# Kernel tuning notes

Hardware: AMD Instinct MI355X
Metric: run time of the kernel (lower is better)

Reference implementation:

```python
import jax, jax.numpy as jnp
import numpy as np

DIM = 384
HEADS = 6
HIDDEN = int(DIM * 4.0)
SQRT_2_OVER_PI = float(np.sqrt(2.0 / np.pi))
LN_EPS = 1e-5


def gelu_tanh(x):
    return 0.5 * x * (1.0 + jnp.tanh(SQRT_2_OVER_PI * (x + 0.044715 * x ** 3)))


def layer_norm(x, g, b):
    m = jnp.mean(x, axis=-1, keepdims=True)
    v = jnp.var(x, axis=-1, keepdims=True)
    return (x - m) * jax.lax.rsqrt(v + LN_EPS) * g + b


def setup_inputs() -> dict:
    key = jax.random.key(0)
    ks = jax.random.split(key, 8)
    s = 0.02
    return {
        "x": jax.random.normal(ks[0], (4, 2048, DIM), dtype=jnp.float32),
        "ln1_g": jnp.ones((DIM,), jnp.float32),
        "ln1_b": jnp.zeros((DIM,), jnp.float32),
        "w_qkv": jax.random.normal(ks[1], (DIM, 3 * DIM), jnp.float32) * s,
        "w_proj": jax.random.normal(ks[2], (DIM, DIM), jnp.float32) * s,
        "b_proj": jnp.zeros((DIM,), jnp.float32),
        "ln2_g": jnp.ones((DIM,), jnp.float32),
        "ln2_b": jnp.zeros((DIM,), jnp.float32),
        "w_fc1": jax.random.normal(ks[3], (DIM, HIDDEN), jnp.float32) * s,
        "b_fc1": jnp.zeros((HIDDEN,), jnp.float32),
        "w_fc2": jax.random.normal(ks[4], (HIDDEN, DIM), jnp.float32) * s,
        "b_fc2": jnp.zeros((DIM,), jnp.float32),
    }


def reference(x, ln1_g, ln1_b, w_qkv, w_proj, b_proj, ln2_g, ln2_b, w_fc1, b_fc1, w_fc2, b_fc2):
    B, N, C = x.shape
    H = HEADS
    Dh = C // H
    scale = Dh ** -0.5

    # Attention (pre-norm)
    h = layer_norm(x, ln1_g, ln1_b)
    qkv = (h @ w_qkv).reshape(B, N, 3, H, Dh)
    q = qkv[:, :, 0].transpose(0, 2, 1, 3)  # [B,H,N,Dh]
    k = qkv[:, :, 1].transpose(0, 2, 1, 3)
    v = qkv[:, :, 2].transpose(0, 2, 1, 3)
    attn = jnp.einsum('bhnd,bhmd->bhnm', q, k) * scale
    attn = jax.nn.softmax(attn, axis=-1)
    o = jnp.einsum('bhnm,bhmd->bhnd', attn, v)
    o = o.transpose(0, 2, 1, 3).reshape(B, N, C)
    x = x + (o @ w_proj + b_proj)

    # MLP (pre-norm)
    h = layer_norm(x, ln2_g, ln2_b)
    h = gelu_tanh(h @ w_fc1 + b_fc1)
    x = x + (h @ w_fc2 + b_fc2)
    return x
```

## Files before the change

### kernel.cpp

```cpp
#include <hip/hip_runtime.h>
#include <hip/hip_bf16.h>
#include <math.h>

#define DIM 384
#define HEADS 6
#define DH 64
#define HIDDEN 1536
#define SEQ 2048
#define NTOK 8192
#define LN_EPS 1e-5f
#define S2PI 0.7978845608028654f
#define KPAD 72

typedef __attribute__((ext_vector_type(8))) short short8;
typedef __attribute__((ext_vector_type(4))) float f32x4;
typedef __attribute__((ext_vector_type(4))) unsigned short ushort4v;
typedef __attribute__((ext_vector_type(8))) unsigned short ushort8v;

#if __has_builtin(__builtin_amdgcn_exp2f)
#define EXP2(x) __builtin_amdgcn_exp2f(x)
#else
#define EXP2(x) exp2f(x)
#endif
#if __has_builtin(__builtin_amdgcn_rcpf)
#define RCPF(x) __builtin_amdgcn_rcpf(x)
#else
#define RCPF(x) (1.f / (x))
#endif

__device__ __forceinline__ unsigned short f2bf(float f) {
    union { float f; unsigned u; } v; v.f = f;
    unsigned r = v.u + 0x7FFFu + ((v.u >> 16) & 1u);
    return (unsigned short)(r >> 16);
}

__device__ __forceinline__ float bf2f(unsigned short u) {
    union { unsigned u; float f; } v; v.u = ((unsigned)u) << 16;
    return v.f;
}

__device__ __forceinline__ float gelu_fast(float v) {
    float u = S2PI * (v + 0.044715f * v * v * v);
    float e = EXP2(u * 2.8853900817779268f);
    return v * (1.f - RCPF(1.f + e));
}

__device__ __forceinline__ void gload16(const unsigned short* g, unsigned short* l) {
    __builtin_amdgcn_global_load_lds(
        (const __attribute__((address_space(1))) unsigned int*)g,
        (__attribute__((address_space(3))) unsigned int*)l, 16, 0, 0);
}

__device__ __forceinline__ void ln_body(const float* __restrict__ x,
                                        const float* __restrict__ g,
                                        const float* __restrict__ b,
                                        unsigned short* __restrict__ out,
                                        int blk, int tid) {
    int row  = blk * 4 + (tid >> 6);
    int lane = tid & 63;
    const float* xr = x + (size_t)row * DIM;
    float v[6];
    float s = 0.f, sq = 0.f;
#pragma unroll
    for (int j = 0; j < 6; ++j) {
        v[j] = xr[lane + 64 * j];
        s += v[j];
        sq += v[j] * v[j];
    }
#pragma unroll
    for (int o = 32; o; o >>= 1) {
        s  += __shfl_xor(s, o);
        sq += __shfl_xor(sq, o);
    }
    float mean = s * (1.f / DIM);
    float var  = sq * (1.f / DIM) - mean * mean;
    float rs   = rsqrtf(var + LN_EPS);
    unsigned short* orow = out + (size_t)row * DIM;
#pragma unroll
    for (int j = 0; j < 6; ++j) {
        int c = lane + 64 * j;
        orow[c] = f2bf((v[j] - mean) * rs * g[c] + b[c]);
    }
}

__device__ __forceinline__ void tr_body(const float* __restrict__ w,
                                        unsigned short* __restrict__ wt,
                                        int K, int N, int bx, int by,
                                        unsigned short (*t)[36], int tid) {
    const int n0 = bx * 32, k0 = by * 32;
    {
        int r = tid >> 3, c4 = (tid & 7) * 4;
        float4 v = *reinterpret_cast<const float4*>(&w[(size_t)(k0 + r) * N + n0 + c4]);
        t[c4 + 0][r] = f2bf(v.x);
        t[c4 + 1][r] = f2bf(v.y);
        t[c4 + 2][r] = f2bf(v.z);
        t[c4 + 3][r] = f2bf(v.w);
    }
    __syncthreads();
    {
        int n = tid >> 3, kk = (tid & 7) * 4;
        ushort4v o = { t[n][kk], t[n][kk + 1], t[n][kk + 2], t[n][kk + 3] };
        *reinterpret_cast<ushort4v*>(&wt[(size_t)(n0 + n) * K + k0 + kk]) = o;
    }
}

__global__ __launch_bounds__(256) void prep_kernel(const float* __restrict__ x,
                                                   const float* __restrict__ g1,
                                                   const float* __restrict__ b1,
                                                   unsigned short* __restrict__ h_bf,
                                                   const float* __restrict__ w_qkv,
                                                   unsigned short* __restrict__ wqkv_t,
                                                   const float* __restrict__ w_proj,
                                                   unsigned short* __restrict__ wproj_t,
                                                   const float* __restrict__ w_fc1,
                                                   unsigned short* __restrict__ wfc1_t,
                                                   const float* __restrict__ w_fc2,
                                                   unsigned short* __restrict__ wfc2_t) {
    __shared__ unsigned short t[32][36];
    const int tid = threadIdx.x;
    int bid = blockIdx.x;
    if (bid < 2048) { ln_body(x, g1, b1, h_bf, bid, tid); return; }
    bid -= 2048;
    if (bid < 432) { tr_body(w_qkv, wqkv_t, DIM, 3 * DIM, bid % 36, bid / 36, t, tid); return; }
    bid -= 432;
    if (bid < 144) { tr_body(w_proj, wproj_t, DIM, DIM, bid % 12, bid / 12, t, tid); return; }
    bid -= 144;
    if (bid < 576) { tr_body(w_fc1, wfc1_t, DIM, HIDDEN, bid % 48, bid / 48, t, tid); return; }
    bid -= 576;
    tr_body(w_fc2, wfc2_t, HIDDEN, DIM, bid % 12, bid / 12, t, tid);
}

__global__ __launch_bounds__(256) void ln_kernel(const float* __restrict__ x,
                                                 const float* __restrict__ g,
                                                 const float* __restrict__ b,
                                                 unsigned short* __restrict__ out) {
    ln_body(x, g, b, out, blockIdx.x, threadIdx.x);
}

template <int EPI, int BN>
__global__ __launch_bounds__(256) void mfma_gemm(const unsigned short* __restrict__ A,
                                                 const unsigned short* __restrict__ Bt,
                                                 const float* __restrict__ bias,
                                                 const float* __restrict__ resid,
                                                 float* __restrict__ Cf,
                                                 unsigned short* __restrict__ Cb,
                                                 unsigned short* __restrict__ Qh,
                                                 unsigned short* __restrict__ Kh,
                                                 unsigned short* __restrict__ Vth,
                                                 int M, int N, int K) {
    constexpr int NF = BN / 32;
    __shared__ __align__(16) unsigned short smem[EPI == 0 ? 17408 : (128 * 64 + BN * 64)];
    unsigned short* As = smem;
    unsigned short* Bs = smem + 128 * 64;

    const int tid = threadIdx.x;
    const int wave = tid >> 6, lane = tid & 63;
    const int lg = lane >> 4, lrr = lane & 15;
    const int wr = wave >> 1, wc = wave & 1;
    const int bm = blockIdx.y * 128, bn = blockIdx.x * BN;

    f32x4 acc[4][NF];
    const f32x4 fzero = {0.f, 0.f, 0.f, 0.f};
#pragma unroll
    for (int m = 0; m < 4; ++m)
#pragma unroll
        for (int n = 0; n < NF; ++n) acc[m][n] = fzero;

    const int grow = wave * 8 + (lane >> 3);
    const int gcol = (lane & 7) * 8;
    const unsigned short* apl = A  + (size_t)(bm + grow) * K + gcol;
    const unsigned short* bpl = Bt + (size_t)(bn + grow) * K + gcol;

    for (int k0 = 0; k0 < K; k0 += 64) {
        __syncthreads();
#pragma unroll
        for (int i = 0; i < 4; ++i)
            gload16(apl + (size_t)(i * 32) * K + k0, As + i * 2048 + wave * 512);
#pragma unroll
        for (int i = 0; i < NF; ++i)
            gload16(bpl + (size_t)(i * 32) * K + k0, Bs + i * 2048 + wave * 512);
        __syncthreads();
#pragma unroll
        for (int s = 0; s < 2; ++s) {
            short8 af[4], bf[NF];
#pragma unroll
            for (int m = 0; m < 4; ++m)
                af[m] = *reinterpret_cast<const short8*>(
                    &As[(wr * 64 + m * 16 + lrr) * 64 + s * 32 + lg * 8]);
#pragma unroll
            for (int n = 0; n < NF; ++n)
                bf[n] = *reinterpret_cast<const short8*>(
                    &Bs[(wc * (BN / 2) + n * 16 + lrr) * 64 + s * 32 + lg * 8]);
#pragma unroll
            for (int m = 0; m < 4; ++m)
#pragma unroll
                for (int n = 0; n < NF; ++n)
                    acc[m][n] = __builtin_amdgcn_mfma_f32_16x16x32_bf16(af[m], bf[n], acc[m][n], 0, 0, 0);
        }
    }

    if (EPI == 1) {
#pragma unroll
        for (int m = 0; m < 4; ++m)
#pragma unroll
            for (int j = 0; j < 4; ++j) {
                int row = bm + wr * 64 + m * 16 + lg * 4 + j;
#pragma unroll
                for (int n = 0; n < NF; ++n) {
                    int col = bn + wc * (BN / 2) + n * 16 + lrr;
                    size_t off = (size_t)row * N + col;
                    Cf[off] = acc[m][n][j] + bias[col] + resid[off];
                }
            }
    } else if (EPI == 2) {
#pragma unroll
        for (int m = 0; m < 4; ++m)
#pragma unroll
            for (int j = 0; j < 4; ++j) {
                int row = bm + wr * 64 + m * 16 + lg * 4 + j;
#pragma unroll
                for (int n = 0; n < NF; ++n) {
                    int col = bn + wc * (BN / 2) + n * 16 + lrr;
                    Cb[(size_t)row * N + col] = f2bf(gelu_fast(acc[m][n][j] + bias[col]));
                }
            }
    } else {
        const int sec = bn / DIM;
        if (sec < 2) {
            unsigned short* dst = (sec == 0) ? Qh : Kh;
#pragma unroll
            for (int m = 0; m < 4; ++m)
#pragma unroll
                for (int j = 0; j < 4; ++j) {
                    int token = bm + wr * 64 + m * 16 + lg * 4 + j;
                    int bb = token >> 11, nn = token & (SEQ - 1);
#pragma unroll
                    for (int n = 0; n < NF; ++n) {
                        int n_glob = bn + wc * (BN / 2) + n * 16 + lrr;
                        int head = (n_glob - sec * DIM) >> 6;
                        int d = n_glob & 63;
                        dst[((size_t)(bb * HEADS + head) * SEQ + nn) * DH + d] =
                            f2bf(acc[m][n][j]);
                    }
                }
        } else {
            __syncthreads();
            unsigned short* T = smem;
#pragma unroll
            for (int m = 0; m < 4; ++m)
#pragma unroll
                for (int n = 0; n < NF; ++n) {
                    int dl = wc * (BN / 2) + n * 16 + lrr;
#pragma unroll
                    for (int j = 0; j < 4; ++j) {
                        int tl = wr * 64 + m * 16 + lg * 4 + j;
                        T[dl * 136 + tl] = f2bf(acc[m][n][j]);
                    }
                }
            __syncthreads();
            int dl = tid >> 1, th = (tid & 1) * 64;
            int dg = bn - 2 * DIM + dl;
            int head = dg >> 6, dd = dg & 63;
            int bb = bm >> 11, nn0 = (bm & (SEQ - 1)) + th;
            unsigned short* dst = &Vth[((size_t)(bb * HEADS + head) * DH + dd) * SEQ + nn0];
#pragma unroll
            for (int i = 0; i < 64; i += 8)
                *reinterpret_cast<ushort8v*>(dst + i) =
                    *reinterpret_cast<const ushort8v*>(&T[dl * 136 + th + i]);
        }
    }
}

__global__ __launch_bounds__(256) void attn_mfma_kernel(const unsigned short* __restrict__ Qh,
                                                        const unsigned short* __restrict__ Kh,
                                                        const unsigned short* __restrict__ Vth,
                                                        unsigned short* __restrict__ out) {
    const int bid = blockIdx.x;
    const int orig = (bid & 7) * 96 + (bid >> 3);
    const int qt = orig & 31;
    const int bh = orig >> 5;
    const int b = bh / HEADS, h = bh % HEADS;
    const int tid = threadIdx.x;
    const int wave = tid >> 6, lane = tid & 63;
    const int lg = lane >> 4;
    const int lrr = lane & 15;

    __shared__ __align__(16) unsigned short Ks[64][KPAD];
    __shared__ __align__(16) unsigned short Vs[64][KPAD];
    __shared__ __align__(16) unsigned short Ps[4][16][KPAD];

    const size_t qkbase = (size_t)bh * SEQ * DH;
    const size_t vbase  = (size_t)bh * DH * SEQ;

    short8 qfrag[2];
    {
        const unsigned short* qp =
            Qh + qkbase + (size_t)(qt * 64 + wave * 16 + lrr) * DH + lg * 8;
        qfrag[0] = *(const short8*)qp;
        qfrag[1] = *(const short8*)(qp + 32);
#pragma unroll
        for (int s = 0; s < 2; ++s)
#pragma unroll
            for (int i = 0; i < 8; ++i)
                qfrag[s][i] = (short)f2bf(bf2f((unsigned short)qfrag[s][i]) * 0.18033688011112042f);
    }

    float lsum = 0.f;
    f32x4 oacc[4];
    const f32x4 fzero = {0.f, 0.f, 0.f, 0.f};
#pragma unroll
    for (int n = 0; n < 4; ++n) oacc[n] = fzero;

    const int sr = tid >> 2;
    const int sc = (tid & 3) * 16;

    const unsigned short* kp = Kh + qkbase + (size_t)sr * DH + sc;
    const unsigned short* vp = Vth + vbase + (size_t)sr * SEQ + sc;
    short8 rk0 = *(const short8*)kp;
    short8 rk1 = *(const short8*)(kp + 8);
    short8 rv0 = *(const short8*)vp;
    short8 rv1 = *(const short8*)(vp + 8);

    const int NT = SEQ / 64;
    for (int kt = 0; kt < NT; ++kt) {
        *(short8*)&Ks[sr][sc]     = rk0;
        *(short8*)&Ks[sr][sc + 8] = rk1;
        *(short8*)&Vs[sr][sc]     = rv0;
        *(short8*)&Vs[sr][sc + 8] = rv1;
        if (kt + 1 < NT) {
            kp += 64 * DH;
            vp += 64;
            rk0 = *(const short8*)kp;
            rk1 = *(const short8*)(kp + 8);
            rv0 = *(const short8*)vp;
            rv1 = *(const short8*)(vp + 8);
        }
        asm volatile("s_waitcnt lgkmcnt(0)" ::: "memory");
        __builtin_amdgcn_s_barrier();
        __builtin_amdgcn_sched_barrier(0);

        f32x4 sacc[4];
#pragma unroll
        for (int ct = 0; ct < 4; ++ct) sacc[ct] = fzero;
        __builtin_amdgcn_s_setprio(1);
#pragma unroll
        for (int ct = 0; ct < 4; ++ct) {
#pragma unroll
            for (int s = 0; s < 2; ++s) {
                short8 kf = *(const short8*)&Ks[ct * 16 + lrr][s * 32 + lg * 8];
                sacc[ct] = __builtin_amdgcn_mfma_f32_16x16x32_bf16(kf, qfrag[s], sacc[ct], 0, 0, 0);
            }
        }
        __builtin_amdgcn_s_setprio(0);

#pragma unroll
        for (int ct = 0; ct < 4; ++ct) {
            float p0 = EXP2(sacc[ct][0]);
            float p1 = EXP2(sacc[ct][1]);
            float p2 = EXP2(sacc[ct][2]);
            float p3 = EXP2(sacc[ct][3]);
            lsum += (p0 + p1) + (p2 + p3);
            union { __hip_bfloat162 h2; unsigned u; } w0, w1;
            w0.h2 = __float22bfloat162_rn(float2{p0, p1});
            w1.h2 = __float22bfloat162_rn(float2{p2, p3});
            unsigned long long dw = (unsigned long long)w0.u |
                                    ((unsigned long long)w1.u << 32);
            *reinterpret_cast<unsigned long long*>(&Ps[wave][lrr][ct * 16 + lg * 4]) = dw;
        }

        short8 pf0 = *(const short8*)&Ps[wave][lrr][lg * 8];
        short8 pf1 = *(const short8*)&Ps[wave][lrr][32 + lg * 8];
        __builtin_amdgcn_s_setprio(1);
#pragma unroll
        for (int n = 0; n < 4; ++n) {
            short8 vf0 = *(const short8*)&Vs[n * 16 + lrr][lg * 8];
            oacc[n] = __builtin_amdgcn_mfma_f32_16x16x32_bf16(pf0, vf0, oacc[n], 0, 0, 0);
            short8 vf1 = *(const short8*)&Vs[n * 16 + lrr][32 + lg * 8];
            oacc[n] = __builtin_amdgcn_mfma_f32_16x16x32_bf16(pf1, vf1, oacc[n], 0, 0, 0);
        }
        __builtin_amdgcn_s_setprio(0);
        __builtin_amdgcn_s_barrier();
    }

    float ls = lsum;
    ls += __shfl_xor(ls, 16);
    ls += __shfl_xor(ls, 32);
    float linv = 1.f / ls;

    const int orow0 = qt * 64 + wave * 16 + lg * 4;
#pragma unroll
    for (int j = 0; j < 4; ++j) {
        float inv = __shfl(linv, lg * 4 + j);
        size_t rowoff = ((size_t)b * SEQ + orow0 + j) * DIM + h * DH + lrr;
#pragma unroll
        for (int n = 0; n < 4; ++n)
            out[rowoff + n * 16] = f2bf(oacc[n][j] * inv);
    }
}

extern "C" void kernel_launch(void* const* d_in, const int* in_sizes, int n_in,
                              void* d_out, int out_size, void* d_ws, size_t ws_size,
                              hipStream_t stream) {
    const float* x      = (const float*)d_in[0];
    const float* ln1_g  = (const float*)d_in[1];
    const float* ln1_b  = (const float*)d_in[2];
    const float* w_qkv  = (const float*)d_in[3];
    const float* w_proj = (const float*)d_in[4];
    const float* b_proj = (const float*)d_in[5];
    const float* ln2_g  = (const float*)d_in[6];
    const float* ln2_b  = (const float*)d_in[7];
    const float* w_fc1  = (const float*)d_in[8];
    const float* b_fc1  = (const float*)d_in[9];
    const float* w_fc2  = (const float*)d_in[10];
    const float* b_fc2  = (const float*)d_in[11];
    float* out = (float*)d_out;

    unsigned short* h_bf   = (unsigned short*)d_ws;
    unsigned short* Qh     = h_bf + (size_t)NTOK * DIM;
    unsigned short* Kh     = Qh + (size_t)NTOK * DIM;
    unsigned short* Vth    = Kh + (size_t)NTOK * DIM;
    unsigned short* fc1_bf = Vth + (size_t)NTOK * DIM;
    unsigned short* wqkv_t = fc1_bf + (size_t)NTOK * HIDDEN;
    unsigned short* wproj_t = wqkv_t + (size_t)DIM * 3 * DIM;
    unsigned short* wfc1_t  = wproj_t + (size_t)DIM * DIM;
    unsigned short* wfc2_t  = wfc1_t + (size_t)DIM * HIDDEN;
    unsigned short* attn_bf = h_bf;
    unsigned short* h2_bf   = Qh;

    prep_kernel<<<3776, 256, 0, stream>>>(x, ln1_g, ln1_b, h_bf,
                                          w_qkv, wqkv_t, w_proj, wproj_t,
                                          w_fc1, wfc1_t, w_fc2, wfc2_t);

    mfma_gemm<0, 128><<<dim3(3 * DIM / 128, NTOK / 128), 256, 0, stream>>>(
        h_bf, wqkv_t, nullptr, nullptr, nullptr, nullptr, Qh, Kh, Vth,
        NTOK, 3 * DIM, DIM);

    attn_mfma_kernel<<<(SEQ / 64) * 4 * HEADS, 256, 0, stream>>>(
        Qh, Kh, Vth, attn_bf);

    mfma_gemm<1, 64><<<dim3(DIM / 64, NTOK / 128), 256, 0, stream>>>(
        attn_bf, wproj_t, b_proj, x, out, nullptr, nullptr, nullptr, nullptr,
        NTOK, DIM, DIM);

    ln_kernel<<<NTOK / 4, 256, 0, stream>>>(out, ln2_g, ln2_b, h2_bf);

    mfma_gemm<2, 128><<<dim3(HIDDEN / 128, NTOK / 128), 256, 0, stream>>>(
        h2_bf, wfc1_t, b_fc1, nullptr, nullptr, fc1_bf, nullptr, nullptr, nullptr,
        NTOK, HIDDEN, DIM);

    mfma_gemm<1, 64><<<dim3(DIM / 64, NTOK / 128), 256, 0, stream>>>(
        fc1_bf, wfc2_t, b_fc2, out, out, nullptr, nullptr, nullptr, nullptr,
        NTOK, DIM, HIDDEN);
}
```

Before: 234.5 us.

## Double-buffer GEMM LDS tiles and XOR-swizzle attention LDS layouts

The GEMM kernel now keeps two LDS buffers and issues the global-to-LDS loads for the next K step before computing on the current one. This is meant to overlap memory latency with MFMA work and removes one barrier per step, at the cost of doubling shared memory. The attention kernel applies an XOR swizzle (16-byte unit XOR row&7) to the K, V and P tiles in LDS to reduce bank conflicts on fragment reads. Row padding is still present, so the swizzle may add address arithmetic without much conflict reduction. The prefetched async LDS loads rely on the barrier at the top of the next iteration for their completion, which could be a correctness risk if that barrier does not wait on vmcnt.

Result: slower. 248.3 us (+5.9%).

```diff
diff --git a/kernel.cpp b/kernel.cpp
--- a/kernel.cpp
+++ b/kernel.cpp
@@ -44,6 +44,8 @@
     float e = EXP2(u * 2.8853900817779268f);
     return v * (1.f - RCPF(1.f + e));
 }
+
+__device__ __forceinline__ int swz(int row, int unit) { return unit ^ (row & 7); }
 
 __device__ __forceinline__ void gload16(const unsigned short* g, unsigned short* l) {
     __builtin_amdgcn_global_load_lds(
@@ -149,9 +151,8 @@
                                                  unsigned short* __restrict__ Vth,
                                                  int M, int N, int K) {
     constexpr int NF = BN / 32;
-    __shared__ __align__(16) unsigned short smem[EPI == 0 ? 17408 : (128 * 64 + BN * 64)];
-    unsigned short* As = smem;
-    unsigned short* Bs = smem + 128 * 64;
+    constexpr int BUFSZ = 128 * 64 + BN * 64;
+    __shared__ __align__(16) unsigned short smem[2 * BUFSZ];
 
     const int tid = threadIdx.x;
     const int wave = tid >> 6, lane = tid & 63;
@@ -171,15 +172,33 @@
     const unsigned short* apl = A  + (size_t)(bm + grow) * K + gcol;
     const unsigned short* bpl = Bt + (size_t)(bn + grow) * K + gcol;
 
-    for (int k0 = 0; k0 < K; k0 += 64) {
+    const int nsteps = K / 64;
+    {
+        unsigned short* As0 = smem;
+        unsigned short* Bs0 = smem + 128 * 64;
+#pragma unroll
+        for (int i = 0; i < 4; ++i)
+            gload16(apl + (size_t)(i * 32) * K, As0 + i * 2048 + wave * 512);
+#pragma unroll
+        for (int i = 0; i < NF; ++i)
+            gload16(bpl + (size_t)(i * 32) * K, Bs0 + i * 2048 + wave * 512);
+    }
+
+    for (int t = 0; t < nsteps; ++t) {
         __syncthreads();
-#pragma unroll
-        for (int i = 0; i < 4; ++i)
-            gload16(apl + (size_t)(i * 32) * K + k0, As + i * 2048 + wave * 512);
-#pragma unroll
-        for (int i = 0; i < NF; ++i)
-            gload16(bpl + (size_t)(i * 32) * K + k0, Bs + i * 2048 + wave * 512);
-        __syncthreads();
+        if (t + 1 < nsteps) {
+            unsigned short* Asn = smem + ((t + 1) & 1) * BUFSZ;
+            unsigned short* Bsn = Asn + 128 * 64;
+            const int k1 = (t + 1) * 64;
+#pragma unroll
+            for (int i = 0; i < 4; ++i)
+                gload16(apl + (size_t)(i * 32) * K + k1, Asn + i * 2048 + wave * 512);
+#pragma unroll
+            for (int i = 0; i < NF; ++i)
+                gload16(bpl + (size_t)(i * 32) * K + k1, Bsn + i * 2048 + wave * 512);
+        }
+        const unsigned short* As = smem + (t & 1) * BUFSZ;
+        const unsigned short* Bs = As + 128 * 64;
 #pragma unroll
         for (int s = 0; s < 2; ++s) {
             short8 af[4], bf[NF];
@@ -312,10 +331,10 @@
     for (int n = 0; n < 4; ++n) oacc[n] = fzero;
 
     const int sr = tid >> 2;
-    const int sc = (tid & 3) * 16;
-
-    const unsigned short* kp = Kh + qkbase + (size_t)sr * DH + sc;
-    const unsigned short* vp = Vth + vbase + (size_t)sr * SEQ + sc;
+    const int u0 = (tid & 3) * 2;
+
+    const unsigned short* kp = Kh + qkbase + (size_t)sr * DH + u0 * 8;
+    const unsigned short* vp = Vth + vbase + (size_t)sr * SEQ + u0 * 8;
     short8 rk0 = *(const short8*)kp;
     short8 rk1 = *(const short8*)(kp + 8);
     short8 rv0 = *(const short8*)vp;
@@ -323,10 +342,10 @@
 
     const int NT = SEQ / 64;
     for (int kt = 0; kt < NT; ++kt) {
-        *(short8*)&Ks[sr][sc]     = rk0;
-        *(short8*)&Ks[sr][sc + 8] = rk1;
-        *(short8*)&Vs[sr][sc]     = rv0;
-        *(short8*)&Vs[sr][sc + 8] = rv1;
+        *(short8*)&Ks[sr][swz(sr, u0) * 8]     = rk0;
+        *(short8*)&Ks[sr][swz(sr, u0 + 1) * 8] = rk1;
+        *(short8*)&Vs[sr][swz(sr, u0) * 8]     = rv0;
+        *(short8*)&Vs[sr][swz(sr, u0 + 1) * 8] = rv1;
         if (kt + 1 < NT) {
             kp += 64 * DH;
             vp += 64;
@@ -347,7 +366,7 @@
         for (int ct = 0; ct < 4; ++ct) {
 #pragma unroll
             for (int s = 0; s < 2; ++s) {
-                short8 kf = *(const short8*)&Ks[ct * 16 + lrr][s * 32 + lg * 8];
+                short8 kf = *(const short8*)&Ks[ct * 16 + lrr][swz(lrr, s * 4 + lg) * 8];
                 sacc[ct] = __builtin_amdgcn_mfma_f32_16x16x32_bf16(kf, qfrag[s], sacc[ct], 0, 0, 0);
             }
         }
@@ -365,17 +384,19 @@
             w1.h2 = __float22bfloat162_rn(float2{p2, p3});
             unsigned long long dw = (unsigned long long)w0.u |
                                     ((unsigned long long)w1.u << 32);
-            *reinterpret_cast<unsigned long long*>(&Ps[wave][lrr][ct * 16 + lg * 4]) = dw;
-        }
-
-        short8 pf0 = *(const short8*)&Ps[wave][lrr][lg * 8];
-        short8 pf1 = *(const short8*)&Ps[wave][lrr][32 + lg * 8];
+            int uq = (ct << 1) | (lg >> 1);
+            *reinterpret_cast<unsigned long long*>(
+                &Ps[wave][lrr][swz(lrr, uq) * 8 + (lg & 1) * 4]) = dw;
+        }
+
+        short8 pf0 = *(const short8*)&Ps[wave][lrr][swz(lrr, lg) * 8];
+        short8 pf1 = *(const short8*)&Ps[wave][lrr][swz(lrr, 4 + lg) * 8];
         __builtin_amdgcn_s_setprio(1);
 #pragma unroll
         for (int n = 0; n < 4; ++n) {
-            short8 vf0 = *(const short8*)&Vs[n * 16 + lrr][lg * 8];
+            short8 vf0 = *(const short8*)&Vs[n * 16 + lrr][swz(lrr, lg) * 8];
             oacc[n] = __builtin_amdgcn_mfma_f32_16x16x32_bf16(pf0, vf0, oacc[n], 0, 0, 0);
-            short8 vf1 = *(const short8*)&Vs[n * 16 + lrr][32 + lg * 8];
+            short8 vf1 = *(const short8*)&Vs[n * 16 + lrr][swz(lrr, 4 + lg) * 8];
             oacc[n] = __builtin_amdgcn_mfma_f32_16x16x32_bf16(pf1, vf1, oacc[n], 0, 0, 0);
         }
         __builtin_amdgcn_s_setprio(0);
```
